# Performance work log

Measured on AMD Instinct MI355X. Metric: run time of the kernel, lower is better.

The kernel has to match this reference:

```python
import jax, jax.numpy as jnp
import numpy as np

N_NODES = 100000
N_EDGES = 1200000
D_IN = 64
D_OUT = 32
BN_EPS = 1e-5


def setup_inputs() -> dict:
    key = jax.random.key(0)
    ks = jax.random.split(key, 8)
    x = jax.random.normal(ks[0], (N_NODES, D_IN), dtype=jnp.float32)
    edge_index = jax.random.randint(ks[1], (2, N_EDGES), 0, N_NODES, dtype=jnp.int64)
    W1s = jax.random.normal(ks[2], (3, D_IN, D_IN), dtype=jnp.float32) * 0.05
    b1s = jax.random.normal(ks[3], (3, D_IN), dtype=jnp.float32) * 0.05
    W2s = jax.random.normal(ks[4], (3, D_IN, D_IN), dtype=jnp.float32) * 0.05
    b2s = jax.random.normal(ks[5], (3, D_IN), dtype=jnp.float32) * 0.05
    gammas = jnp.ones((3, D_IN), dtype=jnp.float32)
    betas = jnp.zeros((3, D_IN), dtype=jnp.float32)
    epss = jnp.zeros((3,), dtype=jnp.float32)  # GINConv train_eps init value 0
    lin_w = jax.random.normal(ks[6], (D_IN, D_OUT), dtype=jnp.float32) * 0.05
    lin_b = jnp.zeros((D_OUT,), dtype=jnp.float32)
    return {"x": x, "edge_index": edge_index, "W1s": W1s, "b1s": b1s,
            "W2s": W2s, "b2s": b2s, "gammas": gammas, "betas": betas,
            "epss": epss, "lin_w": lin_w, "lin_b": lin_b}


def reference(x, edge_index, W1s, b1s, W2s, b2s, gammas, betas, epss, lin_w, lin_b):
    # PyG GINConv (source_to_target): out_i = nn((1+eps)*x_i + sum_{j->i} x_j)
    src = edge_index[0]
    dst = edge_index[1]
    n = x.shape[0]
    h = x
    for i in range(3):
        agg = jax.ops.segment_sum(h[src], dst, num_segments=n)  # [N, d]
        z = (1.0 + epss[i]) * h + agg
        z = jax.nn.relu(z @ W1s[i] + b1s[i])
        z = jax.nn.relu(z @ W2s[i] + b2s[i])
        # BatchNorm1d, training mode (batch statistics, biased variance)
        mu = jnp.mean(z, axis=0)
        var = jnp.var(z, axis=0)
        z = gammas[i] * (z - mu) * jax.lax.rsqrt(var + BN_EPS) + betas[i]
        h = jax.nn.relu(z)  # F.relu after each conv
    return h @ lin_w + lin_b  # [N, D_OUT]
```

## Files before the change

kernel.cpp:

```cpp
#include <hip/hip_runtime.h>
#include <hip/hip_fp16.h>

#define NBMAX 256
#define CHB   7168

typedef _Float16 half8 __attribute__((ext_vector_type(8)));
typedef float f32x4 __attribute__((ext_vector_type(4)));

__device__ __forceinline__ unsigned short f2h(float f) {
    __half h = __float2half_rn(f);
    return *(unsigned short*)&h;
}

__device__ __forceinline__ int scan256(int v, int* wsum, int* woff) {
    int t = threadIdx.x, lane = t & 63, wv = t >> 6;
    int x = v;
    #pragma unroll
    for (int d = 1; d < 64; d <<= 1) {
        int y = __shfl_up(x, d, 64);
        if (lane >= d) x += y;
    }
    if (lane == 63) wsum[wv] = x;
    __syncthreads();
    if (t == 0) {
        int a = 0;
        #pragma unroll
        for (int i = 0; i < 4; ++i) { woff[i] = a; a += wsum[i]; }
    }
    __syncthreads();
    return x - v + woff[wv];
}

__global__ void gin_detect(const void* __restrict__ edge, int* __restrict__ flag, int E) {
    const int* p = (const int*)edge;
    int is64 = 1;
    int m = (E < 64) ? E : 64;
    for (int i = 0; i < m; ++i)
        if (p[2 * i + 1] != 0) is64 = 0;
    *flag = is64;
}

__global__ __launch_bounds__(256) void gin_x16(const float* __restrict__ x,
                                               unsigned short* __restrict__ o, int n16) {
    int i = blockIdx.x * 256 + threadIdx.x;
    if (i >= n16) return;
    float4 v = ((const float4*)x)[i];
    ushort4 u;
    u.x = f2h(v.x); u.y = f2h(v.y); u.z = f2h(v.z); u.w = f2h(v.w);
    ((ushort4*)o)[i] = u;
}

__global__ __launch_bounds__(256) void gin_cbhist(const void* __restrict__ edge,
                                                  const int* __restrict__ flag,
                                                  int* __restrict__ cbcnt, int E, int nb) {
    __shared__ int lc[NBMAX];
    int t = threadIdx.x;
    if (t < nb) lc[t] = 0;
    __syncthreads();
    int is64 = *flag;
    int stride = gridDim.x * 256;
    for (int e = blockIdx.x * 256 + t; e < E; e += stride) {
        int d = is64 ? (int)((const long long*)edge)[E + e] : ((const int*)edge)[E + e];
        atomicAdd(&lc[d >> 9], 1);
    }
    __syncthreads();
    if (t < nb && lc[t]) atomicAdd(&cbcnt[t], lc[t]);
}

__global__ __launch_bounds__(256) void gin_cbscan(const int* __restrict__ cbcnt,
                                                  int* __restrict__ cbbase,
                                                  int* __restrict__ cbcursor, int nb,
                                                  int* __restrict__ rowptr, int n, int E) {
    __shared__ int wsum[4], woff[4];
    int t = threadIdx.x;
    int v = (t < nb) ? cbcnt[t] : 0;
    int excl = scan256(v, wsum, woff);
    if (t < nb) { cbbase[t] = excl; cbcursor[t] = excl; }
    if (t == nb - 1) cbbase[nb] = excl + v;
    if (t == 0) rowptr[n] = E;
}

__global__ __launch_bounds__(256) void gin_binscatter(const void* __restrict__ edge,
                                                      const int* __restrict__ flag,
                                                      int* __restrict__ cbcursor,
                                                      uint2* __restrict__ ebuf, int E, int nb) {
    __shared__ int cnt[NBMAX];
    __shared__ int dlt[NBMAX];
    __shared__ int cur[NBMAX];
    __shared__ int wsum[4], woff[4];
    __shared__ uint2 buf[CHB];
    int t = threadIdx.x;
    int beg = blockIdx.x * CHB;
    int m = E - beg; if (m > CHB) m = CHB;
    if (t < nb) cnt[t] = 0;
    __syncthreads();
    int is64 = *flag;
    for (int j = t; j < m; j += 256) {
        int e = beg + j;
        int d = is64 ? (int)((const long long*)edge)[E + e] : ((const int*)edge)[E + e];
        atomicAdd(&cnt[d >> 9], 1);
    }
    __syncthreads();
    int v = (t < nb) ? cnt[t] : 0;
    int excl = scan256(v, wsum, woff);
    if (t < nb) {
        int gb = v ? atomicAdd(&cbcursor[t], v) : 0;
        dlt[t] = gb - excl;
        cur[t] = excl;
    }
    __syncthreads();
    for (int j = t; j < m; j += 256) {
        int e = beg + j;
        int s, d;
        if (is64) {
            s = (int)((const long long*)edge)[e];
            d = (int)((const long long*)edge)[E + e];
        } else {
            s = ((const int*)edge)[e];
            d = ((const int*)edge)[E + e];
        }
        int p = atomicAdd(&cur[d >> 9], 1);
        buf[p] = make_uint2((unsigned)s, (unsigned)d);
    }
    __syncthreads();
    for (int j = t; j < m; j += 256) {
        uint2 ed = buf[j];
        ebuf[j + dlt[(int)(ed.y >> 9)]] = ed;
    }
}

__global__ __launch_bounds__(256) void gin_build(const uint2* __restrict__ ebuf,
                                                 const int* __restrict__ cbbase,
                                                 int* __restrict__ rowptr,
                                                 int* __restrict__ col, int n) {
    __shared__ int cnt[512];
    __shared__ int off[512];
    __shared__ int wsum[4], woff[4];
    int b = blockIdx.x, t = threadIdx.x;
    int beg = cbbase[b], end = cbbase[b + 1];
    cnt[t] = 0; cnt[t + 256] = 0;
    __syncthreads();
    for (int j = beg + t; j < end; j += 256)
        atomicAdd(&cnt[(int)(ebuf[j].y & 511)], 1);
    __syncthreads();
    int v0 = cnt[2 * t], v1 = cnt[2 * t + 1];
    int ep = scan256(v0 + v1, wsum, woff);
    off[2 * t] = ep;
    off[2 * t + 1] = ep + v0;
    __syncthreads();
    int node0 = b * 512 + 2 * t;
    if (node0 < n) rowptr[node0] = beg + off[2 * t];
    if (node0 + 1 < n) rowptr[node0 + 1] = beg + off[2 * t + 1];
    __syncthreads();
    for (int j = beg + t; j < end; j += 256) {
        uint2 ed = ebuf[j];
        int p = atomicAdd(&off[(int)(ed.y & 511)], 1);
        col[beg + p] = (int)ed.x;
    }
}

template <bool APPLY>
__device__ __forceinline__ void accum8(float* acc, uint4 u,
                                       const float* sc, const float* sh) {
    float v[8];
    float2 f;
    f = __half22float2(*(const __half2*)&u.x); v[0] = f.x; v[1] = f.y;
    f = __half22float2(*(const __half2*)&u.y); v[2] = f.x; v[3] = f.y;
    f = __half22float2(*(const __half2*)&u.z); v[4] = f.x; v[5] = f.y;
    f = __half22float2(*(const __half2*)&u.w); v[6] = f.x; v[7] = f.y;
    #pragma unroll
    for (int j = 0; j < 8; ++j)
        acc[j] += APPLY ? fmaxf(fmaf(v[j], sc[j], sh[j]), 0.f) : v[j];
}

template <bool APPLY>
__device__ __forceinline__ void gather_body(const unsigned short* __restrict__ zb,
                                            const int* __restrict__ rowptr,
                                            const int* __restrict__ col,
                                            const float* __restrict__ epss,
                                            const float* __restrict__ ss,
                                            int layer,
                                            unsigned short* __restrict__ t,
                                            int wid, int l32) {
    int r = l32 >> 3, c = l32 & 7;
    float sc[8] = {1.f, 1.f, 1.f, 1.f, 1.f, 1.f, 1.f, 1.f};
    float sh[8] = {0.f, 0.f, 0.f, 0.f, 0.f, 0.f, 0.f, 0.f};
    if (APPLY) {
        const float* p = ss + (layer - 1) * 128;
        *(float4*)&sc[0] = *(const float4*)(p + 8 * c);
        *(float4*)&sc[4] = *(const float4*)(p + 8 * c + 4);
        *(float4*)&sh[0] = *(const float4*)(p + 64 + 8 * c);
        *(float4*)&sh[4] = *(const float4*)(p + 64 + 8 * c + 4);
    }
    int r0 = rowptr[wid], r1 = rowptr[wid + 1];
    uint4 su = make_uint4(0, 0, 0, 0);
    if (r == 0) su = *(const uint4*)(zb + (size_t)wid * 64 + 8 * c);

    float acc[8] = {0.f, 0.f, 0.f, 0.f, 0.f, 0.f, 0.f, 0.f};
    for (int base = r0; base < r1; base += 16) {
        int i0 = base + r, i1 = i0 + 4, i2 = i0 + 8, i3 = i0 + 12;
        bool p0 = i0 < r1, p1 = i1 < r1, p2 = i2 < r1, p3 = i3 < r1;
        uint4 u0, u1, u2, u3;
        if (p0) u0 = *(const uint4*)(zb + (size_t)col[i0] * 64 + 8 * c);
        if (p1) u1 = *(const uint4*)(zb + (size_t)col[i1] * 64 + 8 * c);
        if (p2) u2 = *(const uint4*)(zb + (size_t)col[i2] * 64 + 8 * c);
        if (p3) u3 = *(const uint4*)(zb + (size_t)col[i3] * 64 + 8 * c);
        if (p0) accum8<APPLY>(acc, u0, sc, sh);
        if (p1) accum8<APPLY>(acc, u1, sc, sh);
        if (p2) accum8<APPLY>(acc, u2, sc, sh);
        if (p3) accum8<APPLY>(acc, u3, sc, sh);
    }
    #pragma unroll
    for (int j = 0; j < 8; ++j) {
        acc[j] += __shfl_xor(acc[j], 8);
        acc[j] += __shfl_xor(acc[j], 16);
    }
    if (r == 0) {
        float e1 = 1.f + epss[layer];
        float s[8];
        float2 f;
        f = __half22float2(*(const __half2*)&su.x); s[0] = f.x; s[1] = f.y;
        f = __half22float2(*(const __half2*)&su.y); s[2] = f.x; s[3] = f.y;
        f = __half22float2(*(const __half2*)&su.z); s[4] = f.x; s[5] = f.y;
        f = __half22float2(*(const __half2*)&su.w); s[6] = f.x; s[7] = f.y;
        #pragma unroll
        for (int j = 0; j < 8; ++j) {
            float v = APPLY ? fmaxf(fmaf(s[j], sc[j], sh[j]), 0.f) : s[j];
            acc[j] = fmaf(e1, v, acc[j]);
        }
        uint4 o;
        o.x = (unsigned)f2h(acc[0]) | ((unsigned)f2h(acc[1]) << 16);
        o.y = (unsigned)f2h(acc[2]) | ((unsigned)f2h(acc[3]) << 16);
        o.z = (unsigned)f2h(acc[4]) | ((unsigned)f2h(acc[5]) << 16);
        o.w = (unsigned)f2h(acc[6]) | ((unsigned)f2h(acc[7]) << 16);
        *(uint4*)(t + (size_t)wid * 64 + 8 * c) = o;
    }
}

__global__ __launch_bounds__(256) void gin_gather(const unsigned short* __restrict__ zb,
                                                  const int* __restrict__ rowptr,
                                                  const int* __restrict__ col,
                                                  const float* __restrict__ epss,
                                                  const float* __restrict__ ss,
                                                  int layer, int apply,
                                                  unsigned short* __restrict__ t, int n) {
    int gw = (blockIdx.x * 256 + threadIdx.x) >> 6;
    int lane = threadIdx.x & 63;
    int wid = gw * 2 + (lane >> 5);
    int l32 = lane & 31;
    if (wid >= n) return;
    if (apply)
        gather_body<true>(zb, rowptr, col, epss, ss, layer, t, wid, l32);
    else
        gather_body<false>(zb, rowptr, col, epss, ss, layer, t, wid, l32);
}

__global__ __launch_bounds__(256) void gin_mlp(const unsigned short* __restrict__ t_in,
                                               unsigned short* __restrict__ z16,
                                               const float* __restrict__ W1g,
                                               const float* __restrict__ b1g,
                                               const float* __restrict__ W2g,
                                               const float* __restrict__ b2g,
                                               float* __restrict__ stats, int layer, int n) {
    __shared__ _Float16 Wt[2 * 64 * 72];
    __shared__ _Float16 Z1[128 * 72];
    __shared__ float sS[64], sQ[64];
    int tid = threadIdx.x;
    int base = blockIdx.x * 128;
    const float* __restrict__ W1 = W1g + layer * 4096;
    const float* __restrict__ W2 = W2g + layer * 4096;

    for (int i = tid; i < 4096; i += 256) {
        int k = i >> 6, nn = i & 63;
        Wt[nn * 72 + k]        = (_Float16)W1[i];
        Wt[4608 + nn * 72 + k] = (_Float16)W2[i];
    }
    if (tid < 64) { sS[tid] = 0.f; sQ[tid] = 0.f; }
    __syncthreads();

    int lane = tid & 63, wv = tid >> 6;
    int g = lane >> 4, q = lane & 15;
    int n0 = 32 * wv + q;
    int n1 = n0 + 16;

    const _Float16* tp = (const _Float16*)t_in + (size_t)base * 64;
    half8 tb00 = *(const half8*)(tp + (size_t)n0 * 64 + 8 * g);
    half8 tb01 = *(const half8*)(tp + (size_t)n0 * 64 + 32 + 8 * g);
    half8 tb10 = *(const half8*)(tp + (size_t)n1 * 64 + 8 * g);
    half8 tb11 = *(const half8*)(tp + (size_t)n1 * 64 + 32 + 8 * g);

    f32x4 acc[2][4];
    #pragma unroll
    for (int nt = 0; nt < 2; ++nt)
        #pragma unroll
        for (int ft = 0; ft < 4; ++ft)
            acc[nt][ft] = (f32x4){0.f, 0.f, 0.f, 0.f};

    #pragma unroll
    for (int ft = 0; ft < 4; ++ft) {
        half8 a0 = *(const half8*)&Wt[(16 * ft + q) * 72 + 8 * g];
        half8 a1 = *(const half8*)&Wt[(16 * ft + q) * 72 + 32 + 8 * g];
        acc[0][ft] = __builtin_amdgcn_mfma_f32_16x16x32_f16(a0, tb00, acc[0][ft], 0, 0, 0);
        acc[0][ft] = __builtin_amdgcn_mfma_f32_16x16x32_f16(a1, tb01, acc[0][ft], 0, 0, 0);
        acc[1][ft] = __builtin_amdgcn_mfma_f32_16x16x32_f16(a0, tb10, acc[1][ft], 0, 0, 0);
        acc[1][ft] = __builtin_amdgcn_mfma_f32_16x16x32_f16(a1, tb11, acc[1][ft], 0, 0, 0);
    }

    #pragma unroll
    for (int ft = 0; ft < 4; ++ft) {
        float4 b = *(const float4*)(b1g + layer * 64 + 16 * ft + 4 * g);
        #pragma unroll
        for (int nt = 0; nt < 2; ++nt) {
            int node = nt ? n1 : n0;
            float v0 = fmaxf(acc[nt][ft][0] + b.x, 0.f);
            float v1 = fmaxf(acc[nt][ft][1] + b.y, 0.f);
            float v2 = fmaxf(acc[nt][ft][2] + b.z, 0.f);
            float v3 = fmaxf(acc[nt][ft][3] + b.w, 0.f);
            uint2 pk;
            pk.x = (unsigned)f2h(v0) | ((unsigned)f2h(v1) << 16);
            pk.y = (unsigned)f2h(v2) | ((unsigned)f2h(v3) << 16);
            *(uint2*)&Z1[node * 72 + 16 * ft + 4 * g] = pk;
        }
    }

    half8 zb00 = *(const half8*)&Z1[n0 * 72 + 8 * g];
    half8 zb01 = *(const half8*)&Z1[n0 * 72 + 32 + 8 * g];
    half8 zb10 = *(const half8*)&Z1[n1 * 72 + 8 * g];
    half8 zb11 = *(const half8*)&Z1[n1 * 72 + 32 + 8 * g];
    #pragma unroll
    for (int nt = 0; nt < 2; ++nt)
        #pragma unroll
        for (int ft = 0; ft < 4; ++ft)
            acc[nt][ft] = (f32x4){0.f, 0.f, 0.f, 0.f};
    #pragma unroll
    for (int ft = 0; ft < 4; ++ft) {
        half8 a0 = *(const half8*)&Wt[4608 + (16 * ft + q) * 72 + 8 * g];
        half8 a1 = *(const half8*)&Wt[4608 + (16 * ft + q) * 72 + 32 + 8 * g];
        acc[0][ft] = __builtin_amdgcn_mfma_f32_16x16x32_f16(a0, zb00, acc[0][ft], 0, 0, 0);
        acc[0][ft] = __builtin_amdgcn_mfma_f32_16x16x32_f16(a1, zb01, acc[0][ft], 0, 0, 0);
        acc[1][ft] = __builtin_amdgcn_mfma_f32_16x16x32_f16(a0, zb10, acc[1][ft], 0, 0, 0);
        acc[1][ft] = __builtin_amdgcn_mfma_f32_16x16x32_f16(a1, zb11, acc[1][ft], 0, 0, 0);
    }

    #pragma unroll
    for (int ft = 0; ft < 4; ++ft) {
        float4 b = *(const float4*)(b2g + layer * 64 + 16 * ft + 4 * g);
        float s[4] = {0.f, 0.f, 0.f, 0.f};
        float sq[4] = {0.f, 0.f, 0.f, 0.f};
        #pragma unroll
        for (int nt = 0; nt < 2; ++nt) {
            int node = base + (nt ? n1 : n0);
            float v0 = fmaxf(acc[nt][ft][0] + b.x, 0.f);
            float v1 = fmaxf(acc[nt][ft][1] + b.y, 0.f);
            float v2 = fmaxf(acc[nt][ft][2] + b.z, 0.f);
            float v3 = fmaxf(acc[nt][ft][3] + b.w, 0.f);
            if (node < n) {
                s[0] += v0; sq[0] += v0 * v0;
                s[1] += v1; sq[1] += v1 * v1;
                s[2] += v2; sq[2] += v2 * v2;
                s[3] += v3; sq[3] += v3 * v3;
                uint2 pk;
                pk.x = (unsigned)f2h(v0) | ((unsigned)f2h(v1) << 16);
                pk.y = (unsigned)f2h(v2) | ((unsigned)f2h(v3) << 16);
                *(uint2*)(z16 + (size_t)node * 64 + 16 * ft + 4 * g) = pk;
            }
        }
        #pragma unroll
        for (int off = 1; off < 16; off <<= 1) {
            #pragma unroll
            for (int r2 = 0; r2 < 4; ++r2) {
                s[r2] += __shfl_xor(s[r2], off);
                sq[r2] += __shfl_xor(sq[r2], off);
            }
        }
        if (q == 0) {
            #pragma unroll
            for (int r2 = 0; r2 < 4; ++r2) {
                atomicAdd(&sS[16 * ft + 4 * g + r2], s[r2]);
                atomicAdd(&sQ[16 * ft + 4 * g + r2], sq[r2]);
            }
        }
    }
    __syncthreads();
    if (tid < 64) {
        atomicAdd(&stats[layer * 128 + tid], sS[tid]);
        atomicAdd(&stats[layer * 128 + 64 + tid], sQ[tid]);
    }
}

__global__ void gin_bnfin(const float* __restrict__ stats, const float* __restrict__ gammas,
                          const float* __restrict__ betas, float* __restrict__ ss,
                          int layer, float n) {
    int f = threadIdx.x;
    float mu = stats[layer * 128 + f] / n;
    float var = stats[layer * 128 + 64 + f] / n - mu * mu;
    float rs = rsqrtf(var + 1e-5f);
    float g = gammas[layer * 64 + f];
    float b = betas[layer * 64 + f];
    ss[layer * 128 + f] = g * rs;
    ss[layer * 128 + 64 + f] = b - g * rs * mu;
}

__global__ __launch_bounds__(256) void gin_lin(const unsigned short* __restrict__ zin,
                                               const float* __restrict__ ss,
                                               const float* __restrict__ lw,
                                               const float* __restrict__ lb,
                                               float* __restrict__ out, int n) {
    __shared__ float Z[128 * 68];
    int tid = threadIdx.x;
    int base = blockIdx.x * 128;
    {
        const ushort4* __restrict__ src = (const ushort4*)(zin + (size_t)base * 64);
        #pragma unroll
        for (int it = 0; it < 8; ++it) {
            int idx4 = it * 256 + tid;
            int row = idx4 >> 4, c = (idx4 & 15) * 4;
            float4 v = make_float4(0.f, 0.f, 0.f, 0.f);
            if (base + row < n) {
                ushort4 u = src[idx4];
                float2 f0 = __half22float2(*(const __half2*)&u.x);
                float2 f1 = __half22float2(*(const __half2*)&u.z);
                v = make_float4(f0.x, f0.y, f1.x, f1.y);
            }
            float4 sc = *(const float4*)(ss + 256 + c);
            float4 sh = *(const float4*)(ss + 256 + 64 + c);
            float4 r;
            r.x = fmaxf(fmaf(v.x, sc.x, sh.x), 0.f);
            r.y = fmaxf(fmaf(v.y, sc.y, sh.y), 0.f);
            r.z = fmaxf(fmaf(v.z, sc.z, sh.z), 0.f);
            r.w = fmaxf(fmaf(v.w, sc.w, sh.w), 0.f);
            *(float4*)&Z[row * 68 + c] = r;
        }
    }
    __syncthreads();
    int tx = tid & 7, ty = tid >> 3;
    float acc[4][4];
    {
        float4 b = *(const float4*)(lb + 4 * tx);
        #pragma unroll
        for (int r = 0; r < 4; ++r) {
            acc[r][0] = b.x; acc[r][1] = b.y; acc[r][2] = b.z; acc[r][3] = b.w;
        }
    }
    #pragma unroll 4
    for (int k = 0; k < 64; ++k) {
        float4 w = *(const float4*)(lw + k * 32 + 4 * tx);
        #pragma unroll
        for (int r = 0; r < 4; ++r) {
            float a = Z[(ty + 32 * r) * 68 + k];
            acc[r][0] = fmaf(a, w.x, acc[r][0]);
            acc[r][1] = fmaf(a, w.y, acc[r][1]);
            acc[r][2] = fmaf(a, w.z, acc[r][2]);
            acc[r][3] = fmaf(a, w.w, acc[r][3]);
        }
    }
    #pragma unroll
    for (int r = 0; r < 4; ++r) {
        int row = base + ty + 32 * r;
        if (row < n) {
            float4 v;
            v.x = acc[r][0]; v.y = acc[r][1]; v.z = acc[r][2]; v.w = acc[r][3];
            *(float4*)(out + (size_t)row * 32 + 4 * tx) = v;
        }
    }
}

extern "C" void kernel_launch(void* const* d_in, const int* in_sizes, int n_in,
                              void* d_out, int out_size, void* d_ws, size_t ws_size,
                              hipStream_t stream) {
    const float* x      = (const float*)d_in[0];
    const void*  edge   = d_in[1];
    const float* W1s    = (const float*)d_in[2];
    const float* b1s    = (const float*)d_in[3];
    const float* W2s    = (const float*)d_in[4];
    const float* b2s    = (const float*)d_in[5];
    const float* gammas = (const float*)d_in[6];
    const float* betas  = (const float*)d_in[7];
    const float* epss   = (const float*)d_in[8];
    const float* lin_w  = (const float*)d_in[9];
    const float* lin_b  = (const float*)d_in[10];
    float* out = (float*)d_out;

    const int N = in_sizes[0] / 64;
    const int E = in_sizes[1] / 2;
    const int NB = (N + 511) >> 9;
    const float fN = (float)N;

    char* w = (char*)d_ws;
    auto take = [&](size_t bytes) {
        char* p = w;
        w += (bytes + 255) & ~(size_t)255;
        return p;
    };
    unsigned short* A  = (unsigned short*)take((size_t)N * 64 * 4);
    unsigned short* zb = (unsigned short*)take((size_t)N * 64 * 2);
    int*   col     = (int*)take((size_t)E * 4);
    int*   rowptr  = (int*)take((size_t)(N + 1) * 4);
    int*   cbcnt   = (int*)take((size_t)NBMAX * 4);
    int*   cbbase  = (int*)take((size_t)(NBMAX + 1) * 4);
    int*   cbcur   = (int*)take((size_t)NBMAX * 4);
    float* stats   = (float*)take(3 * 128 * 4);
    float* ss      = (float*)take(3 * 128 * 4);
    int*   flag    = (int*)take(4);
    uint2*          ebuf = (uint2*)A;
    unsigned short* x16  = zb;

    gin_detect<<<1, 1, 0, stream>>>(edge, flag, E);
    hipMemsetAsync(cbcnt, 0, (size_t)NB * 4, stream);
    hipMemsetAsync(stats, 0, 3 * 128 * 4, stream);
    gin_x16<<<(N * 16 + 255) / 256, 256, 0, stream>>>(x, x16, N * 16);
    gin_cbhist<<<256, 256, 0, stream>>>(edge, flag, cbcnt, E, NB);
    gin_cbscan<<<1, 256, 0, stream>>>(cbcnt, cbbase, cbcur, NB, rowptr, N, E);
    gin_binscatter<<<(E + CHB - 1) / CHB, 256, 0, stream>>>(edge, flag, cbcur, ebuf, E, NB);
    gin_build<<<NB, 256, 0, stream>>>(ebuf, cbbase, rowptr, col, N);

    const int gGather = (N + 7) / 8;
    const int gMlp    = (N + 127) / 128;

    for (int L = 0; L < 3; ++L) {
        const unsigned short* zin = (L == 0) ? x16 : zb;
        gin_gather<<<gGather, 256, 0, stream>>>(zin, rowptr, col, epss, ss, L,
                                                (L > 0) ? 1 : 0, A, N);
        gin_mlp<<<gMlp, 256, 0, stream>>>(A, zb, W1s, b1s, W2s, b2s, stats, L, N);
        gin_bnfin<<<1, 64, 0, stream>>>(stats, gammas, betas, ss, L, fN);
    }
    gin_lin<<<gMlp, 256, 0, stream>>>(zb, ss, lin_w, lin_b, out, N);
}
```

Baseline: 367.3 us.

## Gather with 16 lanes per node and shuffle-broadcast column indices; fuse init memsets

The gather kernel now assigns 16 lanes per destination node instead of 32, so each wave handles four nodes. Each lane loads one column index per 16-edge chunk, and the indices are broadcast with shuffles; each lane then issues eight independent row loads before accumulating. The goal is fewer redundant index loads, more memory requests in flight per lane, and a shorter reduction. Separately, the detect kernel and two memsets are merged into one init kernel to cut launch overhead. The trade-off is higher register use from eight in-flight uint4 loads, and low-degree nodes leave lanes idle.

```diff
diff --git a/kernel.cpp b/kernel.cpp
--- a/kernel.cpp
+++ b/kernel.cpp
@@ -31,13 +31,21 @@
     return x - v + woff[wv];
 }
 
-__global__ void gin_detect(const void* __restrict__ edge, int* __restrict__ flag, int E) {
-    const int* p = (const int*)edge;
-    int is64 = 1;
-    int m = (E < 64) ? E : 64;
-    for (int i = 0; i < m; ++i)
-        if (p[2 * i + 1] != 0) is64 = 0;
-    *flag = is64;
+__global__ __launch_bounds__(256) void gin_init(const void* __restrict__ edge,
+                                                int* __restrict__ flag,
+                                                int* __restrict__ cbcnt, int nb,
+                                                float* __restrict__ stats, int E) {
+    int t = threadIdx.x;
+    for (int i = t; i < nb; i += 256) cbcnt[i] = 0;
+    for (int i = t; i < 384; i += 256) stats[i] = 0.f;
+    if (t == 0) {
+        const int* p = (const int*)edge;
+        int is64 = 1;
+        int m = (E < 64) ? E : 64;
+        for (int i = 0; i < m; ++i)
+            if (p[2 * i + 1] != 0) is64 = 0;
+        *flag = is64;
+    }
 }
 
 __global__ __launch_bounds__(256) void gin_x16(const float* __restrict__ x,
@@ -181,8 +189,8 @@
                                             const float* __restrict__ ss,
                                             int layer,
                                             unsigned short* __restrict__ t,
-                                            int wid, int l32) {
-    int r = l32 >> 3, c = l32 & 7;
+                                            int wid, int qn, int l16) {
+    int r = l16 >> 3, c = l16 & 7;
     float sc[8] = {1.f, 1.f, 1.f, 1.f, 1.f, 1.f, 1.f, 1.f};
     float sh[8] = {0.f, 0.f, 0.f, 0.f, 0.f, 0.f, 0.f, 0.f};
     if (APPLY) {
@@ -198,23 +206,24 @@
 
     float acc[8] = {0.f, 0.f, 0.f, 0.f, 0.f, 0.f, 0.f, 0.f};
     for (int base = r0; base < r1; base += 16) {
-        int i0 = base + r, i1 = i0 + 4, i2 = i0 + 8, i3 = i0 + 12;
-        bool p0 = i0 < r1, p1 = i1 < r1, p2 = i2 < r1, p3 = i3 < r1;
-        uint4 u0, u1, u2, u3;
-        if (p0) u0 = *(const uint4*)(zb + (size_t)col[i0] * 64 + 8 * c);
-        if (p1) u1 = *(const uint4*)(zb + (size_t)col[i1] * 64 + 8 * c);
-        if (p2) u2 = *(const uint4*)(zb + (size_t)col[i2] * 64 + 8 * c);
-        if (p3) u3 = *(const uint4*)(zb + (size_t)col[i3] * 64 + 8 * c);
-        if (p0) accum8<APPLY>(acc, u0, sc, sh);
-        if (p1) accum8<APPLY>(acc, u1, sc, sh);
-        if (p2) accum8<APPLY>(acc, u2, sc, sh);
-        if (p3) accum8<APPLY>(acc, u3, sc, sh);
-    }
-    #pragma unroll
-    for (int j = 0; j < 8; ++j) {
+        int ce = base + l16;
+        int ci = col[ce < r1 ? ce : r1 - 1];
+        uint4 u[8];
+        bool p[8];
+        #pragma unroll
+        for (int s = 0; s < 8; ++s) {
+            int j = 2 * s + r;
+            p[s] = (base + j) < r1;
+            int idx = __shfl(ci, 16 * qn + j);
+            if (p[s]) u[s] = *(const uint4*)(zb + (size_t)idx * 64 + 8 * c);
+        }
+        #pragma unroll
+        for (int s = 0; s < 8; ++s)
+            if (p[s]) accum8<APPLY>(acc, u[s], sc, sh);
+    }
+    #pragma unroll
+    for (int j = 0; j < 8; ++j)
         acc[j] += __shfl_xor(acc[j], 8);
-        acc[j] += __shfl_xor(acc[j], 16);
-    }
     if (r == 0) {
         float e1 = 1.f + epss[layer];
         float s[8];
@@ -246,13 +255,14 @@
                                                   unsigned short* __restrict__ t, int n) {
     int gw = (blockIdx.x * 256 + threadIdx.x) >> 6;
     int lane = threadIdx.x & 63;
-    int wid = gw * 2 + (lane >> 5);
-    int l32 = lane & 31;
+    int qn = lane >> 4;
+    int wid = gw * 4 + qn;
+    int l16 = lane & 15;
     if (wid >= n) return;
     if (apply)
-        gather_body<true>(zb, rowptr, col, epss, ss, layer, t, wid, l32);
+        gather_body<true>(zb, rowptr, col, epss, ss, layer, t, wid, qn, l16);
     else
-        gather_body<false>(zb, rowptr, col, epss, ss, layer, t, wid, l32);
+        gather_body<false>(zb, rowptr, col, epss, ss, layer, t, wid, qn, l16);
 }
 
 __global__ __launch_bounds__(256) void gin_mlp(const unsigned short* __restrict__ t_in,
@@ -505,16 +515,14 @@
     uint2*          ebuf = (uint2*)A;
     unsigned short* x16  = zb;
 
-    gin_detect<<<1, 1, 0, stream>>>(edge, flag, E);
-    hipMemsetAsync(cbcnt, 0, (size_t)NB * 4, stream);
-    hipMemsetAsync(stats, 0, 3 * 128 * 4, stream);
+    gin_init<<<1, 256, 0, stream>>>(edge, flag, cbcnt, NB, stats, E);
     gin_x16<<<(N * 16 + 255) / 256, 256, 0, stream>>>(x, x16, N * 16);
     gin_cbhist<<<256, 256, 0, stream>>>(edge, flag, cbcnt, E, NB);
     gin_cbscan<<<1, 256, 0, stream>>>(cbcnt, cbbase, cbcur, NB, rowptr, N, E);
     gin_binscatter<<<(E + CHB - 1) / CHB, 256, 0, stream>>>(edge, flag, cbcur, ebuf, E, NB);
     gin_build<<<NB, 256, 0, stream>>>(ebuf, cbbase, rowptr, col, N);
 
-    const int gGather = (N + 7) / 8;
+    const int gGather = (N + 15) / 16;
     const int gMlp    = (N + 127) / 128;
 
     for (int L = 0; L < 3; ++L) {
```

New measurement: 346.8 us. -5.6%, faster.
